# Kernel tuning notes

Measured on AMD Instinct MI355X. Metric: run time of the kernel, lower is better.

The kernel has to match this reference:

```python
import jax, jax.numpy as jnp
import numpy as np

INIT_VAL = 2.0
WS = 12
MASK_CONST = -50000.0
EPS = 1.1920929e-07  # torch.finfo(float32).eps


def poolsum(x, b, w, ws):
    """Windowed decay-weighted cumulative pooling, batch_first=False layout.
    x: (T, N, D), b: (T-1, N) in [0,1], w: (T, N) in (0,1].
    """
    T, N, D = x.shape
    dt = x.dtype
    xp = jnp.pad(x, ((ws - 1, 0), (0, 0), (0, 0)))            # (T+ws-1, N, D)
    x_win = jnp.stack([xp[i:i + T] for i in range(ws)], 0)     # (ws, T, N, D); x_win[i,t]=x[t+i-(ws-1)]
    bp = jnp.pad(b, ((ws - 1, 0), (0, 0)))                     # (T+ws-2, N)
    b_win = jnp.stack([bp[i:i + T] for i in range(ws - 1)], 0)  # (ws-1, T, N)
    b_win = jnp.concatenate([b_win, jnp.ones((1, T, N), dt)], 0)  # append ones row -> (ws, T, N)
    # coeffs[i] = prod_{j=i}^{ws-1} b_win[j]  (reverse cumprod)
    coeffs = jnp.flip(jnp.cumprod(jnp.flip(b_win, 0), axis=0), 0)
    wp = jnp.pad(w, ((ws - 1, 0), (0, 0)), constant_values=1.0)
    w_win = jnp.stack([wp[i:i + T] for i in range(ws)], 0)     # (ws, T, N)
    cw = coeffs * w_win
    x_acc = jnp.einsum('wtn,wtnd->tnd', cw, x_win)
    c = cw.sum(0)[..., None]
    return x_acc / c


def _forward(queries, keys, values):
    L, B, KV_H, D = keys.shape
    Q_H = queries.shape[2]
    G = Q_H // KV_H
    k = keys.reshape(L, B * KV_H, D)
    v = values.reshape(L, B * KV_H, D)
    # router on last channel of keys (eval path: straight-through decisions)
    router_logits = k[:, :, -1] - INIT_VAL
    probs = jax.nn.sigmoid(router_logits)
    dec = (probs > 0.5).astype(probs.dtype)
    router_probs = dec - jax.lax.stop_gradient(probs) + probs
    # per-token weights from mean of last channel of grouped query heads
    weight_logits = queries[..., -1].reshape(L, B, KV_H, G).mean(-1).reshape(L, B * KV_H)
    weights = jax.nn.sigmoid(weight_logits + INIT_VAL) + EPS
    pooled = poolsum(jnp.concatenate([k, v], axis=-1), router_probs[1:], weights, WS)
    k2 = pooled[:, :, :D].reshape(L, B, KV_H, D)
    v2 = pooled[:, :, D:].reshape(L, B, KV_H, D)
    rp = router_probs.reshape(L, B, KV_H)
    # eval attn score mask, shifted left by one with zero row appended
    mask = rp * MASK_CONST
    mask = jnp.concatenate([mask[1:], jnp.zeros((1, B, KV_H), mask.dtype)], axis=0)
    # eval path zeroes last channel of q and pooled k
    q_out = queries.at[..., -1].set(0.0)
    k2 = k2.at[..., -1].set(0.0)
    # GQA expansion (optimized_attn_bias=True path)
    k2 = jnp.repeat(k2, G, axis=2)
    v2 = jnp.repeat(v2, G, axis=2)
    mask = jnp.repeat(mask, G, axis=2)
    return q_out, k2, v2, mask


def setup_inputs() -> dict:
    key = jax.random.key(0)
    kq, kk, kv = jax.random.split(key, 3)
    L, B, Q_H, KV_H, D = 2048, 4, 32, 8, 128
    return {
        'queries': jax.random.normal(kq, (L, B, Q_H, D), jnp.float32),
        'keys': jax.random.normal(kk, (L, B, KV_H, D), jnp.float32),
        'values': jax.random.normal(kv, (L, B, KV_H, D), jnp.float32),
    }


def reference(queries, keys, values):
    return _forward(queries, keys, values)
```

## Files before the change

### kernel.cpp

```cpp
#include <hip/hip_runtime.h>
#include <math.h>

#define L 2048
#define B 4
#define QH 32
#define KVH 8
#define G 4
#define D 128
#define NS (B*KVH)
#define WS 12
#define MASK_CONST -50000.0f
#define EPS_F 1.1920929e-07f

#define NQ_BLOCKS   32768
#define NPOOL_BLOCKS 16384
#define NMASK_BLOCKS 1024

typedef float f32x4 __attribute__((ext_vector_type(4)));

__global__ void prep_kernel(const float* __restrict__ q, const float* __restrict__ k,
                            float* __restrict__ dec, float* __restrict__ wts) {
    int idx = blockIdx.x * blockDim.x + threadIdx.x;
    if (idx >= L * NS) return;
    int n = idx & (NS - 1);
    int t = idx / NS;
    float kv = k[(size_t)idx * D + (D - 1)];
    dec[idx] = (kv > 2.0f) ? 1.0f : 0.0f;
    int b = n >> 3, h = n & 7;
    const float* qb = q + (((size_t)t * B + b) * QH + h * G) * D + (D - 1);
    float s = qb[0] + qb[D] + qb[2 * D] + qb[3 * D];
    float logit = s * 0.25f + 2.0f;
    wts[idx] = 1.0f / (1.0f + expf(-logit)) + EPS_F;
}

__global__ void fused_kernel(const f32x4* __restrict__ q4,
                             const float* __restrict__ k, const float* __restrict__ v,
                             const float* __restrict__ dec, const float* __restrict__ wts,
                             f32x4* __restrict__ outq4,
                             float* __restrict__ k2, float* __restrict__ v2,
                             float* __restrict__ mask) {
    int bid = blockIdx.x;
    if (bid < NQ_BLOCKS) {
        size_t i = (size_t)bid * 256 + threadIdx.x;
        f32x4 val = __builtin_nontemporal_load(&q4[i]);
        if ((i & (D / 4 - 1)) == (D / 4 - 1)) val.w = 0.0f;
        __builtin_nontemporal_store(val, &outq4[i]);
    } else if (bid < NQ_BLOCKS + NPOOL_BLOCKS) {
        int pb   = bid - NQ_BLOCKS;
        int grp  = threadIdx.x >> 6;
        int lane = threadIdx.x & 63;
        int pair = pb * 4 + grp;
        int n = pair & (NS - 1);
        int t = pair / NS;
        int c = lane * 4;
        const bool is_k = (c < D);
        const float* base = is_k ? k : v;
        int coff = is_k ? c : (c - D);

        float ax = 0.f, ay = 0.f, az = 0.f, aw = 0.f, den = 0.f;
        float g = 1.f;
        for (int j = 0; j < WS; ++j) {
            int s = t - j;
            if (s < 0) break;
            if (j > 0) {
                g *= dec[(s + 1) * NS + n];
                if (g == 0.f) break;
            }
            float w = wts[s * NS + n];
            const f32x4 x = *reinterpret_cast<const f32x4*>(base + ((size_t)s * NS + n) * D + coff);
            ax += w * x.x; ay += w * x.y; az += w * x.z; aw += w * x.w;
            den += w;
        }
        f32x4 o;
        o.x = ax / den; o.y = ay / den; o.z = az / den; o.w = aw / den;

        int b = n >> 3, h = n & 7;
        size_t head0 = (((size_t)t * B + b) * QH + h * G) * D;
        if (is_k) {
            if (c == D - 4) o.w = 0.0f;
            f32x4* dst = reinterpret_cast<f32x4*>(k2) + (head0 + c) / 4;
            __builtin_nontemporal_store(o, dst);
            __builtin_nontemporal_store(o, dst + D / 4);
            __builtin_nontemporal_store(o, dst + 2 * (D / 4));
            __builtin_nontemporal_store(o, dst + 3 * (D / 4));
        } else {
            f32x4* dst = reinterpret_cast<f32x4*>(v2) + (head0 + (c - D)) / 4;
            __builtin_nontemporal_store(o, dst);
            __builtin_nontemporal_store(o, dst + D / 4);
            __builtin_nontemporal_store(o, dst + 2 * (D / 4));
            __builtin_nontemporal_store(o, dst + 3 * (D / 4));
        }
    } else {
        int idx = (bid - NQ_BLOCKS - NPOOL_BLOCKS) * 256 + threadIdx.x;
        int qh = idx & (QH - 1);
        int b = (idx >> 5) & (B - 1);
        int t = idx >> 7;
        float m = 0.0f;
        if (t < L - 1) m = dec[(t + 1) * NS + b * KVH + (qh >> 2)] * MASK_CONST;
        mask[idx] = m;
    }
}

extern "C" void kernel_launch(void* const* d_in, const int* in_sizes, int n_in,
                              void* d_out, int out_size, void* d_ws, size_t ws_size,
                              hipStream_t stream) {
    const float* q = (const float*)d_in[0];
    const float* k = (const float*)d_in[1];
    const float* v = (const float*)d_in[2];

    float* out_q    = (float*)d_out;
    float* out_k2   = out_q  + (size_t)L * B * QH * D;
    float* out_v2   = out_k2 + (size_t)L * B * QH * D;
    float* out_mask = out_v2 + (size_t)L * B * QH * D;

    float* dec = (float*)d_ws;
    float* wts = dec + (size_t)L * NS;

    {
        int total = L * NS;
        prep_kernel<<<(total + 255) / 256, 256, 0, stream>>>(q, k, dec, wts);
    }
    {
        int blocks = NQ_BLOCKS + NPOOL_BLOCKS + NMASK_BLOCKS;
        fused_kernel<<<blocks, 256, 0, stream>>>(
            (const f32x4*)q, k, v, dec, wts,
            (f32x4*)out_q, out_k2, out_v2, out_mask);
    }
}
```

Baseline: 100.4 us.

## Fold prep kernel into fused kernel, computing router weights per wavefront via shuffles

Removes the separate prep kernel that wrote decision and weight arrays to workspace. Each pooling wavefront now loads the needed query and key last-channel values itself, computes the sigmoid weights and decisions in lanes, and broadcasts them with shuffles. The mask branch reads the key channel directly. This saves a kernel launch and a serialization point, at the cost of redundant scattered loads of q/k last channels across wavefronts.

```diff
diff --git a/kernel.cpp b/kernel.cpp
--- a/kernel.cpp
+++ b/kernel.cpp
@@ -18,24 +18,9 @@
 
 typedef float f32x4 __attribute__((ext_vector_type(4)));
 
-__global__ void prep_kernel(const float* __restrict__ q, const float* __restrict__ k,
-                            float* __restrict__ dec, float* __restrict__ wts) {
-    int idx = blockIdx.x * blockDim.x + threadIdx.x;
-    if (idx >= L * NS) return;
-    int n = idx & (NS - 1);
-    int t = idx / NS;
-    float kv = k[(size_t)idx * D + (D - 1)];
-    dec[idx] = (kv > 2.0f) ? 1.0f : 0.0f;
-    int b = n >> 3, h = n & 7;
-    const float* qb = q + (((size_t)t * B + b) * QH + h * G) * D + (D - 1);
-    float s = qb[0] + qb[D] + qb[2 * D] + qb[3 * D];
-    float logit = s * 0.25f + 2.0f;
-    wts[idx] = 1.0f / (1.0f + expf(-logit)) + EPS_F;
-}
-
 __global__ void fused_kernel(const f32x4* __restrict__ q4,
+                             const float* __restrict__ q,
                              const float* __restrict__ k, const float* __restrict__ v,
-                             const float* __restrict__ dec, const float* __restrict__ wts,
                              f32x4* __restrict__ outq4,
                              float* __restrict__ k2, float* __restrict__ v2,
                              float* __restrict__ mask) {
@@ -51,22 +36,38 @@
         int lane = threadIdx.x & 63;
         int pair = pb * 4 + grp;
         int n = pair & (NS - 1);
-        int t = pair / NS;
+        int t = pair >> 5;
+        int b = n >> 3, h = n & 7;
+
+        float pv = 0.0f;
+        if (lane < 48) {
+            int j = lane >> 2, g = lane & 3;
+            int s = t - j;
+            if (s >= 0)
+                pv = q[(((size_t)s * B + b) * QH + h * G + g) * D + (D - 1)];
+            pv += __shfl_xor(pv, 1);
+            pv += __shfl_xor(pv, 2);
+            pv = 1.0f / (1.0f + __expf(-(pv * 0.25f + 2.0f))) + EPS_F;
+        } else if (lane < 48 + WS - 1) {
+            int u = t - (lane - 48);
+            float kv = (u >= 0) ? k[((size_t)u * NS + n) * D + (D - 1)] : 3.0f;
+            pv = (kv > 2.0f) ? 1.0f : 0.0f;
+        }
+
         int c = lane * 4;
         const bool is_k = (c < D);
         const float* base = is_k ? k : v;
         int coff = is_k ? c : (c - D);
 
         float ax = 0.f, ay = 0.f, az = 0.f, aw = 0.f, den = 0.f;
-        float g = 1.f;
         for (int j = 0; j < WS; ++j) {
             int s = t - j;
             if (s < 0) break;
             if (j > 0) {
-                g *= dec[(s + 1) * NS + n];
-                if (g == 0.f) break;
+                float d = __shfl(pv, 47 + j);
+                if (d == 0.0f) break;
             }
-            float w = wts[s * NS + n];
+            float w = __shfl(pv, 4 * j);
             const f32x4 x = *reinterpret_cast<const f32x4*>(base + ((size_t)s * NS + n) * D + coff);
             ax += w * x.x; ay += w * x.y; az += w * x.z; aw += w * x.w;
             den += w;
@@ -74,7 +75,6 @@
         f32x4 o;
         o.x = ax / den; o.y = ay / den; o.z = az / den; o.w = aw / den;
 
-        int b = n >> 3, h = n & 7;
         size_t head0 = (((size_t)t * B + b) * QH + h * G) * D;
         if (is_k) {
             if (c == D - 4) o.w = 0.0f;
@@ -96,7 +96,11 @@
         int b = (idx >> 5) & (B - 1);
         int t = idx >> 7;
         float m = 0.0f;
-        if (t < L - 1) m = dec[(t + 1) * NS + b * KVH + (qh >> 2)] * MASK_CONST;
+        if (t < L - 1) {
+            int n = b * KVH + (qh >> 2);
+            float kv = k[((size_t)(t + 1) * NS + n) * D + (D - 1)];
+            m = (kv > 2.0f) ? MASK_CONST : 0.0f;
+        }
         mask[idx] = m;
     }
 }
@@ -113,17 +117,8 @@
     float* out_v2   = out_k2 + (size_t)L * B * QH * D;
     float* out_mask = out_v2 + (size_t)L * B * QH * D;
 
-    float* dec = (float*)d_ws;
-    float* wts = dec + (size_t)L * NS;
-
-    {
-        int total = L * NS;
-        prep_kernel<<<(total + 255) / 256, 256, 0, stream>>>(q, k, dec, wts);
-    }
-    {
-        int blocks = NQ_BLOCKS + NPOOL_BLOCKS + NMASK_BLOCKS;
-        fused_kernel<<<blocks, 256, 0, stream>>>(
-            (const f32x4*)q, k, v, dec, wts,
-            (f32x4*)out_q, out_k2, out_v2, out_mask);
-    }
+    int blocks = NQ_BLOCKS + NPOOL_BLOCKS + NMASK_BLOCKS;
+    fused_kernel<<<blocks, 256, 0, stream>>>(
+        (const f32x4*)q, q, k, v,
+        (f32x4*)out_q, out_k2, out_v2, out_mask);
 }
```

Result: slower. 121.8 us (+21.3%).
